# Kernel tuning notes

Measured on AMD Instinct MI355X. Metric: run time of the kernel, lower is better.

## Reference

```python
import jax, jax.numpy as jnp
import numpy as np

N_NODES = 100000
N_EDGES = 3200000
D_FEAT = 256
K_MAX = 5
NEG_SLOPE = 0.2


def _segment_softmax(e, seg, n):
    m = jax.ops.segment_max(e, seg, num_segments=n)
    ex = jnp.exp(e - m[seg])
    s = jax.ops.segment_sum(ex, seg, num_segments=n)
    return ex / (s[seg] + 1e-16)


def setup_inputs() -> dict:
    key = jax.random.key(0)
    ks = jax.random.split(key, 8)
    x = jax.random.normal(ks[0], (N_NODES, D_FEAT), dtype=jnp.float32)
    pos = jax.random.normal(ks[1], (N_NODES, 3), dtype=jnp.float32)
    w_l = jax.random.normal(ks[2], (D_FEAT, 1), dtype=jnp.float32) / np.sqrt(D_FEAT)
    w_r = jax.random.normal(ks[3], (D_FEAT, 1), dtype=jnp.float32) / np.sqrt(D_FEAT)
    w_e = jax.random.normal(ks[4], (3, 1), dtype=jnp.float32)
    att = jax.random.normal(ks[5], (1,), dtype=jnp.float32)
    bias = jnp.zeros((1,), dtype=jnp.float32)
    edge_index = jax.random.randint(ks[6], (2, N_EDGES), 0, N_NODES, dtype=jnp.int64)
    return {"x": x, "pos": pos, "w_l": w_l, "w_r": w_r, "w_e": w_e,
            "att": att, "bias": bias, "edge_index": edge_index}


def reference(x, pos, w_l, w_r, w_e, att, bias, edge_index):
    src, dst = edge_index[0], edge_index[1]
    n = x.shape[0]
    # GATv2Conv (heads=1, out_channels=1) scoring
    xl = x @ w_l                                  # [N,1] source transform
    xr = x @ w_r                                  # [N,1] target transform
    ea = (pos[dst] - pos[src]) @ w_e              # [E,1] edge-attr transform
    msg = xl[src] + xr[dst] + ea                  # [E,1]
    e = (jax.nn.leaky_relu(msg, NEG_SLOPE) * att).sum(-1)  # [E]
    alpha = _segment_softmax(e, dst, n)           # attention over incoming edges
    out = jax.ops.segment_sum(alpha[:, None] * xl[src], dst, num_segments=n) + bias
    logits = out[:, 0]                            # [N]
    score = jax.nn.softmax(logits)                # global node score

    # select highest-score node, grow k-hop neighborhood (<= k_max hops)
    node_id = jnp.argmax(jax.lax.stop_gradient(score))
    reach = jnp.zeros((n,), dtype=bool).at[node_id].set(True)
    for _ in range(K_MAX):
        frontier = jax.ops.segment_max(reach[src].astype(jnp.int32), dst,
                                       num_segments=n) > 0
        reach = reach | frontier
    reach = jax.lax.stop_gradient(reach)

    # pool_val = max over neighborhood features (Neighborhood.pool_val)
    pooled = jnp.max(jnp.where(reach[:, None], x, -jnp.inf), axis=0)  # [D]
    return jnp.concatenate([score, pooled])
```

## Files before the change

kernel.cpp:

```cpp
#include <hip/hip_runtime.h>

#define D_FEAT 256
#define NEG_SLOPE 0.2f
#define MAXBINS 512
#define HISTB 64
#define SENT 0xFFFFFFFFu

__device__ __forceinline__ unsigned fmap(float f) {
    unsigned u = __float_as_uint(f);
    return (u & 0x80000000u) ? ~u : (u | 0x80000000u);
}
__device__ __forceinline__ float funmap(unsigned u) {
    return __uint_as_float((u & 0x80000000u) ? (u ^ 0x80000000u) : ~u);
}


__global__ void k_pre(const float* __restrict__ x, const float* __restrict__ w_l,
                      const float* __restrict__ w_r, const float* __restrict__ pos,
                      const float* __restrict__ w_e,
                      float2* __restrict__ sA, float* __restrict__ Bv,
                      float4* __restrict__ gABpart, unsigned* __restrict__ stampW,
                      unsigned* __restrict__ gHistPart,
                      const int4* __restrict__ dst4, int E4, int nbins,
                      int n, int nW, int gD) {
    int blk = blockIdx.x;
    int tid = threadIdx.x;
    if (blk < gD) {
        int gid = blk * 256 + tid;
        if (gid < nW) stampW[gid] = 0xFFFFFFFFu;
        int w = tid >> 6, lane = tid & 63;
        int node = blk * 4 + w;
        __shared__ float s4[4][4];
        if (node < n) {
            const float4* xv = (const float4*)(x + (size_t)node * D_FEAT);
            float4 v = xv[lane];
            float4 al = ((const float4*)w_l)[lane];
            float4 bl = ((const float4*)w_r)[lane];
            float sl = v.x * al.x + v.y * al.y + v.z * al.z + v.w * al.w;
            float sr = v.x * bl.x + v.y * bl.y + v.z * bl.z + v.w * bl.w;
            #pragma unroll
            for (int o = 32; o; o >>= 1) { sl += __shfl_xor(sl, o); sr += __shfl_xor(sr, o); }
            if (lane == 0) {
                float p = pos[3 * node] * w_e[0] + pos[3 * node + 1] * w_e[1]
                        + pos[3 * node + 2] * w_e[2];
                float a = sl - p;
                float b = sr + p;
                sA[node] = make_float2(a, sl);
                Bv[node] = b;
                s4[w][0] = a; s4[w][1] = b; s4[w][2] = a; s4[w][3] = b;
            }
        } else if (lane == 0) {
            s4[w][0] = -INFINITY; s4[w][1] = -INFINITY;
            s4[w][2] = INFINITY;  s4[w][3] = INFINITY;
        }
        __syncthreads();
        if (tid == 0) {
            float AM = s4[0][0], BM = s4[0][1], Am = s4[0][2], Bm = s4[0][3];
            #pragma unroll
            for (int k = 1; k < 4; ++k) {
                AM = fmaxf(AM, s4[k][0]); BM = fmaxf(BM, s4[k][1]);
                Am = fminf(Am, s4[k][2]); Bm = fminf(Bm, s4[k][3]);
            }
            gABpart[blk] = make_float4(AM, BM, Am, Bm);
        }
    } else {
        int hb = blk - gD;
        __shared__ unsigned h[MAXBINS];
        for (int b = tid; b < nbins; b += 256) h[b] = 0u;
        __syncthreads();
        int stride = HISTB * 256;
        for (int i = hb * 256 + tid; i < E4; i += stride) {
            int4 d = dst4[i];
            atomicAdd(&h[d.x >> 8], 1u);
            atomicAdd(&h[d.y >> 8], 1u);
            atomicAdd(&h[d.z >> 8], 1u);
            atomicAdd(&h[d.w >> 8], 1u);
        }
        __syncthreads();
        for (int b = tid; b < nbins; b += 256) gHistPart[hb * MAXBINS + b] = h[b];
    }
}

__global__ void k_scan2(const float4* __restrict__ gABpart, int nAB,
                        const unsigned* __restrict__ gHistPart,
                        unsigned* __restrict__ gBase, unsigned* __restrict__ gCursor,
                        int nbins, int nBlk, unsigned* sc, const float* __restrict__ att) {
    int tid = threadIdx.x;
    float AM = -INFINITY, BM = -INFINITY, Am = INFINITY, Bm = INFINITY;
    for (int i = tid; i < nAB; i += 256) {
        float4 v = gABpart[i];
        AM = fmaxf(AM, v.x); BM = fmaxf(BM, v.y);
        Am = fminf(Am, v.z); Bm = fminf(Bm, v.w);
    }
    #pragma unroll
    for (int o = 32; o; o >>= 1) {
        AM = fmaxf(AM, __shfl_xor(AM, o)); BM = fmaxf(BM, __shfl_xor(BM, o));
        Am = fminf(Am, __shfl_xor(Am, o)); Bm = fminf(Bm, __shfl_xor(Bm, o));
    }
    __shared__ float s4[4][4];
    int w = tid >> 6, lane = tid & 63;
    if (lane == 0) { s4[w][0] = AM; s4[w][1] = BM; s4[w][2] = Am; s4[w][3] = Bm; }
    __syncthreads();
    if (tid == 0) {
        float am = s4[0][0], bm = s4[0][1], an = s4[0][2], bn = s4[0][3];
        #pragma unroll
        for (int k = 1; k < 4; ++k) {
            am = fmaxf(am, s4[k][0]); bm = fmaxf(bm, s4[k][1]);
            an = fminf(an, s4[k][2]); bn = fminf(bn, s4[k][3]);
        }
        float at = att[0];
        float z = (at >= 0.f) ? (am + bm) : (an + bn);
        float lz = (z >= 0.f) ? z : NEG_SLOPE * z;
        ((float*)sc)[3] = lz * at;
        sc[0] = 0u; ((float*)sc)[1] = 0.f; sc[2] = 0xFFFFFFFFu;
    }
    __shared__ unsigned hs[MAXBINS];
    for (int b = tid; b < nbins; b += 256) {
        unsigned s = 0;
        for (int p = 0; p < HISTB; ++p) s += gHistPart[p * MAXBINS + b];
        hs[b] = s;
    }
    __syncthreads();
    if (tid < 64) {
        unsigned padw = 15u * (unsigned)nBlk;
        unsigned carry = 0;
        for (int b0 = 0; b0 < nbins; b0 += 64) {
            int b = b0 + tid;
            unsigned v = (b < nbins) ? ((hs[b] + padw + 15u) & ~15u) : 0u;
            unsigned inc = v;
            #pragma unroll
            for (int o = 1; o < 64; o <<= 1) {
                unsigned t = __shfl_up(inc, o);
                if (tid >= o) inc += t;
            }
            unsigned excl = inc - v + carry;
            if (b < nbins) { gBase[b] = excl; gCursor[b] = excl; }
            carry += __shfl(inc, 63);
        }
    }
}

__global__ void k_scatter(const int4* __restrict__ src4, const int4* __restrict__ dst4,
                          unsigned* __restrict__ gCursor, unsigned* __restrict__ recs,
                          int E4, int nbins) {
    __shared__ unsigned h[MAXBINS];
    __shared__ unsigned base[MAXBINS];
    for (int b = threadIdx.x; b < nbins; b += 512) h[b] = 0u;
    __syncthreads();
    int b4 = blockIdx.x * 4096;
    #pragma unroll
    for (int g = 0; g < 8; ++g) {
        int idx = b4 + g * 512 + threadIdx.x;
        if (idx < E4) {
            int4 d = dst4[idx];
            atomicAdd(&h[d.x >> 8], 1u);
            atomicAdd(&h[d.y >> 8], 1u);
            atomicAdd(&h[d.z >> 8], 1u);
            atomicAdd(&h[d.w >> 8], 1u);
        }
    }
    __syncthreads();
    for (int b = threadIdx.x; b < nbins; b += 512) {
        unsigned c = h[b];
        h[b] = 0u;
        base[b] = c ? atomicAdd(&gCursor[b], (c + 15u) & ~15u) : 0u;
    }
    __syncthreads();
    #pragma unroll
    for (int g = 0; g < 8; ++g) {
        int idx = b4 + g * 512 + threadIdx.x;
        if (idx < E4) {
            int4 sv = src4[idx];
            int4 dv = dst4[idx];
            int ss[4] = { sv.x, sv.y, sv.z, sv.w };
            int dd[4] = { dv.x, dv.y, dv.z, dv.w };
            #pragma unroll
            for (int j = 0; j < 4; ++j) {
                int d_ = dd[j];
                int bin = d_ >> 8;
                unsigned off = atomicAdd(&h[bin], 1u);
                recs[base[bin] + off] = (unsigned)ss[j] | ((unsigned)(d_ & 255) << 17);
            }
        }
    }
    __syncthreads();
    for (int b = threadIdx.x; b < nbins; b += 512) {
        unsigned c = h[b];
        unsigned pc = (c + 15u) & ~15u;
        for (unsigned k = c; k < pc; ++k) recs[base[b] + k] = SENT;
    }
}

__global__ void k_binsum(const uint4* __restrict__ recs4, const unsigned* __restrict__ gBase,
                         const unsigned* __restrict__ gCursor,
                         const float2* __restrict__ sA, const float* __restrict__ Bv,
                         const float* __restrict__ att, const float* __restrict__ bias,
                         float* __restrict__ logits, unsigned* sc, int n) {
    __shared__ float accx[256];
    __shared__ float accy[256];
    __shared__ float Bb[256];
    int b = blockIdx.x;
    int tid = threadIdx.x;
    int node0 = b << 8;
    accx[tid] = 0.f; accy[tid] = 0.f;
    Bb[tid] = (node0 + tid < n) ? Bv[node0 + tid] : 0.f;
    __syncthreads();
    const float at = att[0];
    const float M = ((const float*)sc)[3];
    unsigned q0 = gBase[b] >> 2, q1 = gCursor[b] >> 2;
    for (unsigned i = q0 + tid; i < q1; i += 256u) {
        uint4 r4 = recs4[i];
        unsigned ws[4] = { r4.x, r4.y, r4.z, r4.w };
        #pragma unroll
        for (int j = 0; j < 4; ++j) {
            unsigned wv = ws[j];
            if (wv == SENT) continue;
            int sidx = (int)(wv & 0x1FFFFu);
            int loc  = (int)(wv >> 17);
            float2 sa = sA[sidx];
            float msg = sa.x + Bb[loc];
            float lr = (msg >= 0.f) ? msg : NEG_SLOPE * msg;
            float e = expf(lr * at - M);
            atomicAdd(&accx[loc], e);
            atomicAdd(&accy[loc], e * sa.y);
        }
    }
    __syncthreads();
    int node = node0 + tid;
    float lg = -INFINITY;
    if (node < n) {
        lg = accy[tid] / (accx[tid] + 1e-38f) + bias[0];
        logits[node] = lg;
    }
    unsigned mu = fmap(lg);
    #pragma unroll
    for (int o = 32; o; o >>= 1) { unsigned t = __shfl_xor(mu, o); mu = (t > mu) ? t : mu; }
    __shared__ unsigned wm[4];
    int w_ = tid >> 6, l = tid & 63;
    if (l == 0) wm[w_] = mu;
    __syncthreads();
    if (tid == 0) {
        unsigned m = wm[0];
        #pragma unroll
        for (int k = 1; k < 4; ++k) m = (wm[k] > m) ? wm[k] : m;
        atomicMax(&sc[0], m);
    }
}


__global__ void k_sumarg(const float* __restrict__ logits, unsigned* sc, int n) {
    int i = blockIdx.x * blockDim.x + threadIdx.x;
    unsigned gmax_u = sc[0];
    float gmax = funmap(gmax_u);
    float ex = 0.f;
    if (i < n) {
        float lg = logits[i];
        ex = expf(lg - gmax);
        if (fmap(lg) == gmax_u) atomicMin(&sc[2], (unsigned)i);
    }
    #pragma unroll
    for (int o = 32; o; o >>= 1) ex += __shfl_xor(ex, o);
    if ((threadIdx.x & 63) == 0) atomicAdd((float*)&sc[1], ex);
}

__global__ void k_score(const float* __restrict__ logits, const unsigned* __restrict__ sc,
                        float* __restrict__ out, unsigned char* stamp, int n) {
    int i = blockIdx.x * blockDim.x + threadIdx.x;
    if (i >= n) return;
    float gmax = funmap(sc[0]);
    float gsum = ((const float*)sc)[1];
    out[i] = expf(logits[i] - gmax) / gsum;
    if (i == (int)sc[2]) stamp[i] = 0;
}

__global__ void k_bfs_rec(const uint4* __restrict__ recs4, const unsigned* __restrict__ gBase,
                          const unsigned* __restrict__ gCursor,
                          unsigned char* __restrict__ stamp, int n, int t) {
    __shared__ unsigned char st[256];
    __shared__ unsigned char mark[256];
    __shared__ unsigned char wn[4];
    int b = blockIdx.x;
    int tid = threadIdx.x;
    int node = (b << 8) + tid;
    unsigned char th = (unsigned char)t;
    unsigned char s = (node < n) ? stamp[node] : (unsigned char)0;
    st[tid] = s; mark[tid] = 0;
    unsigned long long ball = __ballot(s > th);
    if ((tid & 63) == 0) wn[tid >> 6] = (ball != 0ull) ? 1 : 0;
    __syncthreads();
    if (!(wn[0] | wn[1] | wn[2] | wn[3])) return;
    unsigned q0 = gBase[b] >> 2, q1 = gCursor[b] >> 2;
    for (unsigned i = q0 + tid; i < q1; i += 256u) {
        uint4 r4 = recs4[i];
        unsigned ws[4] = { r4.x, r4.y, r4.z, r4.w };
        #pragma unroll
        for (int j = 0; j < 4; ++j) {
            unsigned wv = ws[j];
            if (wv == SENT) continue;
            int loc = (int)(wv >> 17);
            if (st[loc] > th) {
                if (stamp[wv & 0x1FFFFu] < th) mark[loc] = 1;
            }
        }
    }
    __syncthreads();
    if (mark[tid] && node < n && st[tid] > th) stamp[node] = th;
}

__global__ void k_pool1(const float* __restrict__ x, const unsigned char* __restrict__ stamp,
                        float4* __restrict__ partial, int n) {
    int sub = threadIdx.x >> 6;
    int lane = threadIdx.x & 63;
    float4 m = make_float4(-INFINITY, -INFINITY, -INFINITY, -INFINITY);
    int stride = gridDim.x * 4;
    for (int node = blockIdx.x * 4 + sub; node < n; node += stride) {
        if (stamp[node] != 0xFF) {
            float4 v = ((const float4*)(x + (size_t)node * D_FEAT))[lane];
            m.x = fmaxf(m.x, v.x); m.y = fmaxf(m.y, v.y);
            m.z = fmaxf(m.z, v.z); m.w = fmaxf(m.w, v.w);
        }
    }
    __shared__ float4 red[256];
    red[threadIdx.x] = m;
    __syncthreads();
    if (sub == 0) {
        float4 a = red[lane], b = red[64 + lane], c = red[128 + lane], d = red[192 + lane];
        a.x = fmaxf(fmaxf(a.x, b.x), fmaxf(c.x, d.x));
        a.y = fmaxf(fmaxf(a.y, b.y), fmaxf(c.y, d.y));
        a.z = fmaxf(fmaxf(a.z, b.z), fmaxf(c.z, d.z));
        a.w = fmaxf(fmaxf(a.w, b.w), fmaxf(c.w, d.w));
        partial[(size_t)blockIdx.x * 64 + lane] = a;
    }
}

__global__ void k_pool2f(const float4* __restrict__ partial, int nblk1,
                         float* __restrict__ out, int n) {
    int sub = threadIdx.x >> 6;
    int lane = threadIdx.x & 63;
    float4 m = make_float4(-INFINITY, -INFINITY, -INFINITY, -INFINITY);
    for (int r = sub; r < nblk1; r += 4) {
        float4 v = partial[(size_t)r * 64 + lane];
        m.x = fmaxf(m.x, v.x); m.y = fmaxf(m.y, v.y);
        m.z = fmaxf(m.z, v.z); m.w = fmaxf(m.w, v.w);
    }
    __shared__ float4 red[256];
    red[threadIdx.x] = m;
    __syncthreads();
    if (sub == 0) {
        float4 a = red[lane], b = red[64 + lane], c = red[128 + lane], d = red[192 + lane];
        a.x = fmaxf(fmaxf(a.x, b.x), fmaxf(c.x, d.x));
        a.y = fmaxf(fmaxf(a.y, b.y), fmaxf(c.y, d.y));
        a.z = fmaxf(fmaxf(a.z, b.z), fmaxf(c.z, d.z));
        a.w = fmaxf(fmaxf(a.w, b.w), fmaxf(c.w, d.w));
        out[n + 4 * lane + 0] = a.x;
        out[n + 4 * lane + 1] = a.y;
        out[n + 4 * lane + 2] = a.z;
        out[n + 4 * lane + 3] = a.w;
    }
}


__global__ void k_init(float2* NS, unsigned* stampW, int nW, unsigned* pooled_u,
                       unsigned* sc, int n) {
    int i = blockIdx.x * blockDim.x + threadIdx.x;
    if (i < n) NS[i] = make_float2(0.f, 0.f);
    if (i < nW) stampW[i] = 0xFFFFFFFFu;
    if (i < D_FEAT) pooled_u[i] = 0u;
    if (i == 0) {
        sc[0] = 0u; ((float*)sc)[1] = 0.f; sc[2] = 0xFFFFFFFFu;
        sc[4] = 0u; sc[5] = 0u; sc[6] = 0xFFFFFFFFu; sc[7] = 0xFFFFFFFFu;
    }
}

__global__ void k_dots(const float* __restrict__ x, const float* __restrict__ w_l,
                       const float* __restrict__ w_r, float* __restrict__ xl,
                       float* __restrict__ xr, int n) {
    int wave = (int)((blockIdx.x * blockDim.x + threadIdx.x) >> 6);
    int lane = threadIdx.x & 63;
    if (wave >= n) return;
    const float4* xv = (const float4*)(x + (size_t)wave * D_FEAT);
    float4 v = xv[lane];
    float4 a = ((const float4*)w_l)[lane];
    float4 b = ((const float4*)w_r)[lane];
    float sl = v.x * a.x + v.y * a.y + v.z * a.z + v.w * a.w;
    float sr = v.x * b.x + v.y * b.y + v.z * b.z + v.w * b.w;
    #pragma unroll
    for (int o = 32; o; o >>= 1) { sl += __shfl_xor(sl, o); sr += __shfl_xor(sr, o); }
    if (lane == 0) { xl[wave] = sl; xr[wave] = sr; }
}

__global__ void k_ab(const float* __restrict__ xl, const float* __restrict__ xr,
                     const float* __restrict__ pos, const float* __restrict__ w_e,
                     float2* __restrict__ sA, float* __restrict__ B,
                     unsigned* sc, int n) {
    int i = blockIdx.x * blockDim.x + threadIdx.x;
    float amax, amin, bmax, bmin;
    if (i < n) {
        float p = pos[3 * i] * w_e[0] + pos[3 * i + 1] * w_e[1] + pos[3 * i + 2] * w_e[2];
        float xli = xl[i];
        float a = xli - p;
        float b = xr[i] + p;
        sA[i] = make_float2(a, xli);
        B[i] = b;
        amax = amin = a; bmax = bmin = b;
    } else {
        amax = bmax = -INFINITY; amin = bmin = INFINITY;
    }
    #pragma unroll
    for (int o = 32; o; o >>= 1) {
        amax = fmaxf(amax, __shfl_xor(amax, o));
        bmax = fmaxf(bmax, __shfl_xor(bmax, o));
        amin = fminf(amin, __shfl_xor(amin, o));
        bmin = fminf(bmin, __shfl_xor(bmin, o));
    }
    __shared__ float s4[4][4];
    int w = threadIdx.x >> 6, l = threadIdx.x & 63;
    if (l == 0) { s4[w][0] = amax; s4[w][1] = bmax; s4[w][2] = amin; s4[w][3] = bmin; }
    __syncthreads();
    if (threadIdx.x == 0) {
        float AM = s4[0][0], BM = s4[0][1], Am = s4[0][2], Bm = s4[0][3];
        #pragma unroll
        for (int k = 1; k < 4; ++k) {
            AM = fmaxf(AM, s4[k][0]); BM = fmaxf(BM, s4[k][1]);
            Am = fminf(Am, s4[k][2]); Bm = fminf(Bm, s4[k][3]);
        }
        atomicMax(&sc[4], fmap(AM)); atomicMax(&sc[5], fmap(BM));
        atomicMin(&sc[6], fmap(Am)); atomicMin(&sc[7], fmap(Bm));
    }
}

__global__ void k_scanM(unsigned* sc, const float* __restrict__ att) {
    if (threadIdx.x == 0) {
        float at = att[0];
        float z = (at >= 0.f) ? (funmap(sc[4]) + funmap(sc[5]))
                              : (funmap(sc[6]) + funmap(sc[7]));
        float lz = (z >= 0.f) ? z : NEG_SLOPE * z;
        ((float*)sc)[3] = lz * at;
        sc[0] = 0u; ((float*)sc)[1] = 0.f; sc[2] = 0xFFFFFFFFu;
    }
}

__global__ void k_edge_sum(const int* __restrict__ src, const int* __restrict__ dst,
                           const float2* __restrict__ sA, const float* __restrict__ B,
                           const float* __restrict__ att, const unsigned* __restrict__ sc,
                           float2* NS, int E) {
    int i = blockIdx.x * blockDim.x + threadIdx.x;
    if (i >= E) return;
    int s = src[i], d = dst[i];
    float2 sa = sA[s];
    float msg = sa.x + B[d];
    float lr = (msg >= 0.f) ? msg : NEG_SLOPE * msg;
    float ex = expf(lr * att[0] - ((const float*)sc)[3]);
    atomicAdd(&NS[d].x, ex);
    atomicAdd(&NS[d].y, ex * sa.y);
}

__global__ void k_logits(const float2* __restrict__ NS, const float* __restrict__ bias,
                         float* __restrict__ logits, unsigned* sc, int n) {
    int i = blockIdx.x * blockDim.x + threadIdx.x;
    unsigned mu = 0u;
    if (i < n) {
        float2 ns = NS[i];
        float lg = ns.y / (ns.x + 1e-38f) + bias[0];
        logits[i] = lg;
        mu = fmap(lg);
    }
    #pragma unroll
    for (int o = 32; o; o >>= 1) { unsigned t = __shfl_xor(mu, o); mu = (t > mu) ? t : mu; }
    if ((threadIdx.x & 63) == 0) atomicMax(&sc[0], mu);
}

__global__ void k_bfs_stamp(const int4* __restrict__ src4, const int4* __restrict__ dst4,
                            unsigned char* __restrict__ stamp, int E4, int t) {
    int i = blockIdx.x * blockDim.x + threadIdx.x;
    if (i >= E4) return;
    int4 s = src4[i];
    unsigned char th = (unsigned char)t;
    bool h0 = stamp[s.x] < th;
    bool h1 = stamp[s.y] < th;
    bool h2 = stamp[s.z] < th;
    bool h3 = stamp[s.w] < th;
    if (!(h0 | h1 | h2 | h3)) return;
    int4 d = dst4[i];
    if (h0 && stamp[d.x] > th) stamp[d.x] = th;
    if (h1 && stamp[d.y] > th) stamp[d.y] = th;
    if (h2 && stamp[d.z] > th) stamp[d.z] = th;
    if (h3 && stamp[d.w] > th) stamp[d.w] = th;
}

__global__ void k_pool2(const float4* __restrict__ partial, int nblk1, unsigned* pooled_u) {
    int sub = threadIdx.x >> 6;
    int lane = threadIdx.x & 63;
    int chunk = (nblk1 + gridDim.x - 1) / gridDim.x;
    int b0 = blockIdx.x * chunk;
    int b1 = min(b0 + chunk, nblk1);
    float4 m = make_float4(-INFINITY, -INFINITY, -INFINITY, -INFINITY);
    for (int b = b0 + sub; b < b1; b += 4) {
        float4 v = partial[(size_t)b * 64 + lane];
        m.x = fmaxf(m.x, v.x); m.y = fmaxf(m.y, v.y);
        m.z = fmaxf(m.z, v.z); m.w = fmaxf(m.w, v.w);
    }
    __shared__ float4 red[256];
    red[threadIdx.x] = m;
    __syncthreads();
    if (sub == 0) {
        float4 a = red[lane], b = red[64 + lane], c = red[128 + lane], d = red[192 + lane];
        a.x = fmaxf(fmaxf(a.x, b.x), fmaxf(c.x, d.x));
        a.y = fmaxf(fmaxf(a.y, b.y), fmaxf(c.y, d.y));
        a.z = fmaxf(fmaxf(a.z, b.z), fmaxf(c.z, d.z));
        a.w = fmaxf(fmaxf(a.w, b.w), fmaxf(c.w, d.w));
        atomicMax(&pooled_u[lane * 4 + 0], fmap(a.x));
        atomicMax(&pooled_u[lane * 4 + 1], fmap(a.y));
        atomicMax(&pooled_u[lane * 4 + 2], fmap(a.z));
        atomicMax(&pooled_u[lane * 4 + 3], fmap(a.w));
    }
}

__global__ void k_poolwrite(const unsigned* __restrict__ pooled_u, float* __restrict__ out, int n) {
    int t = threadIdx.x;
    out[n + t] = funmap(pooled_u[t]);
}

extern "C" void kernel_launch(void* const* d_in, const int* in_sizes, int n_in,
                              void* d_out, int out_size, void* d_ws, size_t ws_size,
                              hipStream_t stream) {
    const float* x    = (const float*)d_in[0];
    const float* pos  = (const float*)d_in[1];
    const float* w_l  = (const float*)d_in[2];
    const float* w_r  = (const float*)d_in[3];
    const float* w_e  = (const float*)d_in[4];
    const float* att  = (const float*)d_in[5];
    const float* bias = (const float*)d_in[6];
    const int*   ei   = (const int*)d_in[7];

    const int n = in_sizes[0] / D_FEAT;
    const int E = in_sizes[7] / 2;
    const int* src = ei;
    const int* dst = ei + E;
    const int nbins = (n + 255) >> 8;
    const int nW = (n + 3) / 4;
    const int nBlkScat = (E + 16383) / 16384;
    const int Bk = 256;
    const int gN  = (n + Bk - 1) / Bk;
    const int gE  = (E + Bk - 1) / Bk;
    const int gD  = (n + 3) / 4;
    const int E4  = E / 4;
    const int gE4 = (E4 + Bk - 1) / Bk;

    float* f0 = (float*)d_ws;
    size_t o = 0;
    float*    xl       = f0 + o; o += (size_t)n;
    float*    xr       = f0 + o; o += (size_t)n;
    float2*   sA       = (float2*)(f0 + o); o += 2 * (size_t)n;
    float*    B        = f0 + o; o += (size_t)n;
    float*    logits   = f0 + o; o += (size_t)n;
    o = (o + 3) & ~(size_t)3;
    float2*   NS       = (float2*)(f0 + o); o += 2 * (size_t)n;
    float4*   partialF = (float4*)NS;
    unsigned* stampW   = (unsigned*)(f0 + o); o += (size_t)nW;
    unsigned char* stamp = (unsigned char*)stampW;
    unsigned* pooled_u = (unsigned*)(f0 + o); o += 256;
    unsigned* sc       = (unsigned*)(f0 + o); o += 64;
    unsigned* gBase    = (unsigned*)(f0 + o); o += MAXBINS;
    unsigned* gCursor  = (unsigned*)(f0 + o); o += MAXBINS;
    o = (o + 3) & ~(size_t)3;
    float4*   gABpart  = (float4*)(f0 + o); o += 4 * (size_t)gD;
    unsigned* gHistPart= (unsigned*)(f0 + o); o += (size_t)HISTB * MAXBINS;
    o = (o + 15) & ~(size_t)15;
    unsigned* recs     = (unsigned*)(f0 + o);
    float4*   partialT = (float4*)recs;

    size_t capWords = (size_t)E + (size_t)nbins * (15u * (size_t)nBlkScat + 16u);
    size_t need_bytes = (o + capWords) * sizeof(float);
    const bool sorted_ok = (ws_size >= need_bytes) && (nbins <= MAXBINS) &&
                           (E % 4 == 0) && (n <= (1 << 17));

    float* out = (float*)d_out;

    if (sorted_ok) {
        k_pre<<<gD + HISTB, Bk, 0, stream>>>(x, w_l, w_r, pos, w_e, sA, B, gABpart,
                                             stampW, gHistPart, (const int4*)dst,
                                             E4, nbins, n, nW, gD);
        k_scan2<<<1, Bk, 0, stream>>>(gABpart, gD, gHistPart, gBase, gCursor,
                                      nbins, nBlkScat, sc, att);
        k_scatter<<<nBlkScat, 512, 0, stream>>>((const int4*)src, (const int4*)dst,
                                                gCursor, recs, E4, nbins);
        k_binsum<<<nbins, Bk, 0, stream>>>((const uint4*)recs, gBase, gCursor, sA, B,
                                           att, bias, logits, sc, n);
        k_sumarg<<<gN, Bk, 0, stream>>>(logits, sc, n);
        k_score<<<gN, Bk, 0, stream>>>(logits, sc, out, stamp, n);
        for (int t = 1; t <= 5; ++t) {
            k_bfs_rec<<<nbins, Bk, 0, stream>>>((const uint4*)recs, gBase, gCursor,
                                                stamp, n, t);
        }
        k_pool1<<<768, Bk, 0, stream>>>(x, stamp, partialT, n);
        k_pool2f<<<1, Bk, 0, stream>>>(partialT, 768, out, n);
    } else {
        k_init<<<gN, Bk, 0, stream>>>(NS, stampW, nW, pooled_u, sc, n);
        k_dots<<<gD, Bk, 0, stream>>>(x, w_l, w_r, xl, xr, n);
        k_ab<<<gN, Bk, 0, stream>>>(xl, xr, pos, w_e, sA, B, sc, n);
        k_scanM<<<1, 64, 0, stream>>>(sc, att);
        k_edge_sum<<<gE, Bk, 0, stream>>>(src, dst, sA, B, att, sc, NS, E);
        k_logits<<<gN, Bk, 0, stream>>>(NS, bias, logits, sc, n);
        k_sumarg<<<gN, Bk, 0, stream>>>(logits, sc, n);
        k_score<<<gN, Bk, 0, stream>>>(logits, sc, out, stamp, n);
        for (int t = 1; t <= 5; ++t) {
            k_bfs_stamp<<<gE4, Bk, 0, stream>>>((const int4*)src, (const int4*)dst,
                                                stamp, E4, t);
        }
        int nblk1 = (int)((2 * (size_t)n) / 256);
        if (nblk1 > 768) nblk1 = 768;
        if (nblk1 < 1) nblk1 = 1;
        k_pool1<<<nblk1, Bk, 0, stream>>>(x, stamp, partialF, n);
        k_pool2<<<16, Bk, 0, stream>>>(partialF, nblk1, pooled_u);
        k_poolwrite<<<1, Bk, 0, stream>>>(pooled_u, out, n);
    }
}
```

Before: 328.5 us.

## Split histogram into own kernel, batch node dots, fuse pool reduction with last-block

The node projection kernel now handles four nodes per wavefront with independent loads, and the edge histogram moves to its own 512-block kernel that accumulates straight into one global histogram with atomics, so the scan no longer sums 64 partial histograms. The pooling kernel loads two rows per iteration without waiting on the stamp check, and a last-block-done counter folds the second pooling reduction into the same launch. These changes aim to cut launch count, reduction overhead and load latency. The cost is an extra launch for the histogram, unconditional reads of unreached rows in pooling, and a dependency on the stamp-init ordering and the sc[8] counter reset.

Result: slower. 339.4 us (+3.3%).

```diff
diff --git a/kernel.cpp b/kernel.cpp
--- a/kernel.cpp
+++ b/kernel.cpp
@@ -3,7 +3,6 @@
 #define D_FEAT 256
 #define NEG_SLOPE 0.2f
 #define MAXBINS 512
-#define HISTB 64
 #define SENT 0xFFFFFFFFu
 
 __device__ __forceinline__ unsigned fmap(float f) {
@@ -12,6 +11,9 @@
 }
 __device__ __forceinline__ float funmap(unsigned u) {
     return __uint_as_float((u & 0x80000000u) ? (u ^ 0x80000000u) : ~u);
+}
+__device__ __forceinline__ float dot4(float4 v, float4 w) {
+    return v.x * w.x + v.y * w.y + v.z * w.z + v.w * w.w;
 }
 
 
@@ -20,69 +22,103 @@
                       const float* __restrict__ w_e,
                       float2* __restrict__ sA, float* __restrict__ Bv,
                       float4* __restrict__ gABpart, unsigned* __restrict__ stampW,
-                      unsigned* __restrict__ gHistPart,
-                      const int4* __restrict__ dst4, int E4, int nbins,
-                      int n, int nW, int gD) {
-    int blk = blockIdx.x;
-    int tid = threadIdx.x;
-    if (blk < gD) {
-        int gid = blk * 256 + tid;
-        if (gid < nW) stampW[gid] = 0xFFFFFFFFu;
-        int w = tid >> 6, lane = tid & 63;
-        int node = blk * 4 + w;
-        __shared__ float s4[4][4];
-        if (node < n) {
-            const float4* xv = (const float4*)(x + (size_t)node * D_FEAT);
-            float4 v = xv[lane];
-            float4 al = ((const float4*)w_l)[lane];
-            float4 bl = ((const float4*)w_r)[lane];
-            float sl = v.x * al.x + v.y * al.y + v.z * al.z + v.w * al.w;
-            float sr = v.x * bl.x + v.y * bl.y + v.z * bl.z + v.w * bl.w;
-            #pragma unroll
-            for (int o = 32; o; o >>= 1) { sl += __shfl_xor(sl, o); sr += __shfl_xor(sr, o); }
-            if (lane == 0) {
-                float p = pos[3 * node] * w_e[0] + pos[3 * node + 1] * w_e[1]
-                        + pos[3 * node + 2] * w_e[2];
-                float a = sl - p;
-                float b = sr + p;
-                sA[node] = make_float2(a, sl);
-                Bv[node] = b;
-                s4[w][0] = a; s4[w][1] = b; s4[w][2] = a; s4[w][3] = b;
-            }
-        } else if (lane == 0) {
-            s4[w][0] = -INFINITY; s4[w][1] = -INFINITY;
-            s4[w][2] = INFINITY;  s4[w][3] = INFINITY;
-        }
-        __syncthreads();
-        if (tid == 0) {
-            float AM = s4[0][0], BM = s4[0][1], Am = s4[0][2], Bm = s4[0][3];
-            #pragma unroll
-            for (int k = 1; k < 4; ++k) {
-                AM = fmaxf(AM, s4[k][0]); BM = fmaxf(BM, s4[k][1]);
-                Am = fminf(Am, s4[k][2]); Bm = fminf(Bm, s4[k][3]);
-            }
-            gABpart[blk] = make_float4(AM, BM, Am, Bm);
-        }
-    } else {
-        int hb = blk - gD;
-        __shared__ unsigned h[MAXBINS];
-        for (int b = tid; b < nbins; b += 256) h[b] = 0u;
-        __syncthreads();
-        int stride = HISTB * 256;
-        for (int i = hb * 256 + tid; i < E4; i += stride) {
-            int4 d = dst4[i];
-            atomicAdd(&h[d.x >> 8], 1u);
-            atomicAdd(&h[d.y >> 8], 1u);
-            atomicAdd(&h[d.z >> 8], 1u);
-            atomicAdd(&h[d.w >> 8], 1u);
-        }
-        __syncthreads();
-        for (int b = tid; b < nbins; b += 256) gHistPart[hb * MAXBINS + b] = h[b];
-    }
+                      unsigned* __restrict__ gHist, int n, int nW) {
+    int blk = blockIdx.x, tid = threadIdx.x;
+    int gid = blk * 256 + tid;
+    if (gid < nW) stampW[gid] = 0xFFFFFFFFu;
+    if (blk == 0) {
+        if (tid < MAXBINS) gHist[tid] = 0u;
+        if (tid + 256 < MAXBINS) gHist[tid + 256] = 0u;
+    }
+    int w = tid >> 6, lane = tid & 63;
+    int node0 = blk * 16 + w * 4;
+    float4 al = ((const float4*)w_l)[lane];
+    float4 bl = ((const float4*)w_r)[lane];
+    float sl0 = 0.f, sl1 = 0.f, sl2 = 0.f, sl3 = 0.f;
+    float sr0 = 0.f, sr1 = 0.f, sr2 = 0.f, sr3 = 0.f;
+    if (node0 + 3 < n) {
+        float4 v0 = ((const float4*)(x + (size_t)node0 * D_FEAT))[lane];
+        float4 v1 = ((const float4*)(x + (size_t)(node0 + 1) * D_FEAT))[lane];
+        float4 v2 = ((const float4*)(x + (size_t)(node0 + 2) * D_FEAT))[lane];
+        float4 v3 = ((const float4*)(x + (size_t)(node0 + 3) * D_FEAT))[lane];
+        sl0 = dot4(v0, al); sr0 = dot4(v0, bl);
+        sl1 = dot4(v1, al); sr1 = dot4(v1, bl);
+        sl2 = dot4(v2, al); sr2 = dot4(v2, bl);
+        sl3 = dot4(v3, al); sr3 = dot4(v3, bl);
+    } else if (node0 < n) {
+        if (node0 < n) {
+            float4 v = ((const float4*)(x + (size_t)node0 * D_FEAT))[lane];
+            sl0 = dot4(v, al); sr0 = dot4(v, bl);
+        }
+        if (node0 + 1 < n) {
+            float4 v = ((const float4*)(x + (size_t)(node0 + 1) * D_FEAT))[lane];
+            sl1 = dot4(v, al); sr1 = dot4(v, bl);
+        }
+        if (node0 + 2 < n) {
+            float4 v = ((const float4*)(x + (size_t)(node0 + 2) * D_FEAT))[lane];
+            sl2 = dot4(v, al); sr2 = dot4(v, bl);
+        }
+    }
+    #pragma unroll
+    for (int o = 32; o; o >>= 1) {
+        sl0 += __shfl_xor(sl0, o); sr0 += __shfl_xor(sr0, o);
+        sl1 += __shfl_xor(sl1, o); sr1 += __shfl_xor(sr1, o);
+        sl2 += __shfl_xor(sl2, o); sr2 += __shfl_xor(sr2, o);
+        sl3 += __shfl_xor(sl3, o); sr3 += __shfl_xor(sr3, o);
+    }
+    float amax = -INFINITY, bmaxv = -INFINITY, amin = INFINITY, bminv = INFINITY;
+    int node = node0 + lane;
+    if (lane < 4 && node < n) {
+        float slv = (lane == 0) ? sl0 : (lane == 1) ? sl1 : (lane == 2) ? sl2 : sl3;
+        float srv = (lane == 0) ? sr0 : (lane == 1) ? sr1 : (lane == 2) ? sr2 : sr3;
+        float p = pos[3 * node] * w_e[0] + pos[3 * node + 1] * w_e[1]
+                + pos[3 * node + 2] * w_e[2];
+        float a = slv - p, b = srv + p;
+        sA[node] = make_float2(a, slv);
+        Bv[node] = b;
+        amax = a; amin = a; bmaxv = b; bminv = b;
+    }
+    #pragma unroll
+    for (int o = 1; o < 4; o <<= 1) {
+        amax = fmaxf(amax, __shfl_xor(amax, o));
+        bmaxv = fmaxf(bmaxv, __shfl_xor(bmaxv, o));
+        amin = fminf(amin, __shfl_xor(amin, o));
+        bminv = fminf(bminv, __shfl_xor(bminv, o));
+    }
+    __shared__ float s4[4][4];
+    if (lane == 0) { s4[w][0] = amax; s4[w][1] = bmaxv; s4[w][2] = amin; s4[w][3] = bminv; }
+    __syncthreads();
+    if (tid == 0) {
+        float AM = s4[0][0], BM = s4[0][1], Am = s4[0][2], Bm = s4[0][3];
+        #pragma unroll
+        for (int k = 1; k < 4; ++k) {
+            AM = fmaxf(AM, s4[k][0]); BM = fmaxf(BM, s4[k][1]);
+            Am = fminf(Am, s4[k][2]); Bm = fminf(Bm, s4[k][3]);
+        }
+        gABpart[blk] = make_float4(AM, BM, Am, Bm);
+    }
+}
+
+__global__ void k_hist(const int4* __restrict__ dst4, int E4, int nbins,
+                       unsigned* __restrict__ gHist) {
+    __shared__ unsigned h[MAXBINS];
+    for (int b = threadIdx.x; b < nbins; b += blockDim.x) h[b] = 0u;
+    __syncthreads();
+    int stride = gridDim.x * blockDim.x;
+    for (int i = blockIdx.x * blockDim.x + threadIdx.x; i < E4; i += stride) {
+        int4 d = dst4[i];
+        atomicAdd(&h[d.x >> 8], 1u);
+        atomicAdd(&h[d.y >> 8], 1u);
+        atomicAdd(&h[d.z >> 8], 1u);
+        atomicAdd(&h[d.w >> 8], 1u);
+    }
+    __syncthreads();
+    for (int b = threadIdx.x; b < nbins; b += blockDim.x)
+        if (h[b]) atomicAdd(&gHist[b], h[b]);
 }
 
 __global__ void k_scan2(const float4* __restrict__ gABpart, int nAB,
-                        const unsigned* __restrict__ gHistPart,
+                        const unsigned* __restrict__ gHist,
                         unsigned* __restrict__ gBase, unsigned* __restrict__ gCursor,
                         int nbins, int nBlk, unsigned* sc, const float* __restrict__ att) {
     int tid = threadIdx.x;
@@ -112,13 +148,7 @@
         float z = (at >= 0.f) ? (am + bm) : (an + bn);
         float lz = (z >= 0.f) ? z : NEG_SLOPE * z;
         ((float*)sc)[3] = lz * at;
-        sc[0] = 0u; ((float*)sc)[1] = 0.f; sc[2] = 0xFFFFFFFFu;
-    }
-    __shared__ unsigned hs[MAXBINS];
-    for (int b = tid; b < nbins; b += 256) {
-        unsigned s = 0;
-        for (int p = 0; p < HISTB; ++p) s += gHistPart[p * MAXBINS + b];
-        hs[b] = s;
+        sc[0] = 0u; ((float*)sc)[1] = 0.f; sc[2] = 0xFFFFFFFFu; sc[8] = 0u;
     }
     __syncthreads();
     if (tid < 64) {
@@ -126,7 +156,7 @@
         unsigned carry = 0;
         for (int b0 = 0; b0 < nbins; b0 += 64) {
             int b = b0 + tid;
-            unsigned v = (b < nbins) ? ((hs[b] + padw + 15u) & ~15u) : 0u;
+            unsigned v = (b < nbins) ? ((gHist[b] + padw + 15u) & ~15u) : 0u;
             unsigned inc = v;
             #pragma unroll
             for (int o = 1; o < 64; o <<= 1) {
@@ -307,17 +337,27 @@
     if (mark[tid] && node < n && st[tid] > th) stamp[node] = th;
 }
 
-__global__ void k_pool1(const float* __restrict__ x, const unsigned char* __restrict__ stamp,
-                        float4* __restrict__ partial, int n) {
+__global__ void k_pool1f(const float* __restrict__ x, const unsigned char* __restrict__ stamp,
+                         float4* __restrict__ partial, float* __restrict__ out,
+                         unsigned* sc, int nblk, int n) {
     int sub = threadIdx.x >> 6;
     int lane = threadIdx.x & 63;
     float4 m = make_float4(-INFINITY, -INFINITY, -INFINITY, -INFINITY);
-    int stride = gridDim.x * 4;
-    for (int node = blockIdx.x * 4 + sub; node < n; node += stride) {
-        if (stamp[node] != 0xFF) {
-            float4 v = ((const float4*)(x + (size_t)node * D_FEAT))[lane];
-            m.x = fmaxf(m.x, v.x); m.y = fmaxf(m.y, v.y);
-            m.z = fmaxf(m.z, v.z); m.w = fmaxf(m.w, v.w);
+    int stride = gridDim.x * 8;
+    for (int node = blockIdx.x * 8 + sub * 2; node < n; node += stride) {
+        float4 va = ((const float4*)(x + (size_t)node * D_FEAT))[lane];
+        bool hb = (node + 1) < n;
+        float4 vb = va;
+        if (hb) vb = ((const float4*)(x + (size_t)(node + 1) * D_FEAT))[lane];
+        bool ra = stamp[node] != 0xFF;
+        bool rb = hb && (stamp[node + 1] != 0xFF);
+        if (ra) {
+            m.x = fmaxf(m.x, va.x); m.y = fmaxf(m.y, va.y);
+            m.z = fmaxf(m.z, va.z); m.w = fmaxf(m.w, va.w);
+        }
+        if (rb) {
+            m.x = fmaxf(m.x, vb.x); m.y = fmaxf(m.y, vb.y);
+            m.z = fmaxf(m.z, vb.z); m.w = fmaxf(m.w, vb.w);
         }
     }
     __shared__ float4 red[256];
@@ -331,20 +371,20 @@
         a.w = fmaxf(fmaxf(a.w, b.w), fmaxf(c.w, d.w));
         partial[(size_t)blockIdx.x * 64 + lane] = a;
     }
-}
-
-__global__ void k_pool2f(const float4* __restrict__ partial, int nblk1,
-                         float* __restrict__ out, int n) {
-    int sub = threadIdx.x >> 6;
-    int lane = threadIdx.x & 63;
-    float4 m = make_float4(-INFINITY, -INFINITY, -INFINITY, -INFINITY);
-    for (int r = sub; r < nblk1; r += 4) {
+    __threadfence();
+    __shared__ int isLast;
+    if (threadIdx.x == 0) isLast = (atomicAdd(&sc[8], 1u) == (unsigned)(nblk - 1)) ? 1 : 0;
+    __syncthreads();
+    if (!isLast) return;
+    __threadfence();
+    float4 m2 = make_float4(-INFINITY, -INFINITY, -INFINITY, -INFINITY);
+    for (int r = sub; r < nblk; r += 4) {
         float4 v = partial[(size_t)r * 64 + lane];
-        m.x = fmaxf(m.x, v.x); m.y = fmaxf(m.y, v.y);
-        m.z = fmaxf(m.z, v.z); m.w = fmaxf(m.w, v.w);
-    }
-    __shared__ float4 red[256];
-    red[threadIdx.x] = m;
+        m2.x = fmaxf(m2.x, v.x); m2.y = fmaxf(m2.y, v.y);
+        m2.z = fmaxf(m2.z, v.z); m2.w = fmaxf(m2.w, v.w);
+    }
+    __syncthreads();
+    red[threadIdx.x] = m2;
     __syncthreads();
     if (sub == 0) {
         float4 a = red[lane], b = red[64 + lane], c = red[128 + lane], d = red[192 + lane];
@@ -382,8 +422,8 @@
     float4 v = xv[lane];
     float4 a = ((const float4*)w_l)[lane];
     float4 b = ((const float4*)w_r)[lane];
-    float sl = v.x * a.x + v.y * a.y + v.z * a.z + v.w * a.w;
-    float sr = v.x * b.x + v.y * b.y + v.z * b.z + v.w * b.w;
+    float sl = dot4(v, a);
+    float sr = dot4(v, b);
     #pragma unroll
     for (int o = 32; o; o >>= 1) { sl += __shfl_xor(sl, o); sr += __shfl_xor(sr, o); }
     if (lane == 0) { xl[wave] = sl; xr[wave] = sr; }
@@ -488,6 +528,32 @@
     if (h3 && stamp[d.w] > th) stamp[d.w] = th;
 }
 
+__global__ void k_pool1(const float* __restrict__ x, const unsigned char* __restrict__ stamp,
+                        float4* __restrict__ partial, int n) {
+    int sub = threadIdx.x >> 6;
+    int lane = threadIdx.x & 63;
+    float4 m = make_float4(-INFINITY, -INFINITY, -INFINITY, -INFINITY);
+    int stride = gridDim.x * 4;
+    for (int node = blockIdx.x * 4 + sub; node < n; node += stride) {
+        if (stamp[node] != 0xFF) {
+            float4 v = ((const float4*)(x + (size_t)node * D_FEAT))[lane];
+            m.x = fmaxf(m.x, v.x); m.y = fmaxf(m.y, v.y);
+            m.z = fmaxf(m.z, v.z); m.w = fmaxf(m.w, v.w);
+        }
+    }
+    __shared__ float4 red[256];
+    red[threadIdx.x] = m;
+    __syncthreads();
+    if (sub == 0) {
+        float4 a = red[lane], b = red[64 + lane], c = red[128 + lane], d = red[192 + lane];
+        a.x = fmaxf(fmaxf(a.x, b.x), fmaxf(c.x, d.x));
+        a.y = fmaxf(fmaxf(a.y, b.y), fmaxf(c.y, d.y));
+        a.z = fmaxf(fmaxf(a.z, b.z), fmaxf(c.z, d.z));
+        a.w = fmaxf(fmaxf(a.w, b.w), fmaxf(c.w, d.w));
+        partial[(size_t)blockIdx.x * 64 + lane] = a;
+    }
+}
+
 __global__ void k_pool2(const float4* __restrict__ partial, int nblk1, unsigned* pooled_u) {
     int sub = threadIdx.x >> 6;
     int lane = threadIdx.x & 63;
@@ -544,6 +610,7 @@
     const int gN  = (n + Bk - 1) / Bk;
     const int gE  = (E + Bk - 1) / Bk;
     const int gD  = (n + 3) / 4;
+    const int gP  = (n + 15) / 16;
     const int E4  = E / 4;
     const int gE4 = (E4 + Bk - 1) / Bk;
 
@@ -563,9 +630,9 @@
     unsigned* sc       = (unsigned*)(f0 + o); o += 64;
     unsigned* gBase    = (unsigned*)(f0 + o); o += MAXBINS;
     unsigned* gCursor  = (unsigned*)(f0 + o); o += MAXBINS;
+    unsigned* gHist    = (unsigned*)(f0 + o); o += MAXBINS;
     o = (o + 3) & ~(size_t)3;
-    float4*   gABpart  = (float4*)(f0 + o); o += 4 * (size_t)gD;
-    unsigned* gHistPart= (unsigned*)(f0 + o); o += (size_t)HISTB * MAXBINS;
+    float4*   gABpart  = (float4*)(f0 + o); o += 4 * (size_t)gP;
     o = (o + 15) & ~(size_t)15;
     unsigned* recs     = (unsigned*)(f0 + o);
     float4*   partialT = (float4*)recs;
@@ -578,10 +645,10 @@
     float* out = (float*)d_out;
 
     if (sorted_ok) {
-        k_pre<<<gD + HISTB, Bk, 0, stream>>>(x, w_l, w_r, pos, w_e, sA, B, gABpart,
-                                             stampW, gHistPart, (const int4*)dst,
-                                             E4, nbins, n, nW, gD);
-        k_scan2<<<1, Bk, 0, stream>>>(gABpart, gD, gHistPart, gBase, gCursor,
+        k_pre<<<gP, Bk, 0, stream>>>(x, w_l, w_r, pos, w_e, sA, B, gABpart,
+                                     stampW, gHist, n, nW);
+        k_hist<<<512, Bk, 0, stream>>>((const int4*)dst, E4, nbins, gHist);
+        k_scan2<<<1, Bk, 0, stream>>>(gABpart, gP, gHist, gBase, gCursor,
                                       nbins, nBlkScat, sc, att);
         k_scatter<<<nBlkScat, 512, 0, stream>>>((const int4*)src, (const int4*)dst,
                                                 gCursor, recs, E4, nbins);
@@ -593,8 +660,7 @@
             k_bfs_rec<<<nbins, Bk, 0, stream>>>((const uint4*)recs, gBase, gCursor,
                                                 stamp, n, t);
         }
-        k_pool1<<<768, Bk, 0, stream>>>(x, stamp, partialT, n);
-        k_pool2f<<<1, Bk, 0, stream>>>(partialT, 768, out, n);
+        k_pool1f<<<768, Bk, 0, stream>>>(x, stamp, partialT, out, sc, 768, n);
     } else {
         k_init<<<gN, Bk, 0, stream>>>(NS, stampW, nW, pooled_u, sc, n);
         k_dots<<<gD, Bk, 0, stream>>>(x, w_l, w_r, xl, xr, n);
```
